# Kernel tuning notes

Measured on AMD Instinct MI355X. Metric: run time of the kernel, lower is better.

## Reference

```python
import jax, jax.numpy as jnp
import numpy as np

N_EV, N_CS, N_TR, N_ENV = 40000, 30000, 20000, 10000
N = N_EV + N_CS + N_TR + N_ENV  # 100000 nodes
E = 3_200_000                   # edges (avg degree 32)
FEAT, HID = 32, 64
N_GRAPHS, NPG = 100, 1000       # 100 graphs of 1000 nodes


def _p(k, shape, scale=0.1):
    return (jax.random.normal(k, shape, jnp.float32) * scale)


def setup_inputs() -> dict:
    key = jax.random.key(0)
    ks = jax.random.split(key, 24)
    inp = {
        'ev_features': jax.random.normal(ks[0], (N_EV, 6), jnp.float32),
        'cs_features': jax.random.normal(ks[1], (N_CS, 4), jnp.float32),
        'tr_features': jax.random.normal(ks[2], (N_TR, 2), jnp.float32),
        'env_features': jax.random.normal(ks[3], (N_ENV, 5), jnp.float32),
        'edge_index': jax.random.randint(ks[4], (2, E), 0, N, jnp.int32),
        'ev_indexes': jnp.arange(0, N_EV, dtype=jnp.int32),
        'cs_indexes': jnp.arange(N_EV, N_EV + N_CS, dtype=jnp.int32),
        'tr_indexes': jnp.arange(N_EV + N_CS, N_EV + N_CS + N_TR, dtype=jnp.int32),
        'env_indexes': jnp.arange(N - N_ENV, N, dtype=jnp.int32),
        'batch': (jnp.arange(N, dtype=jnp.int32) // NPG),
        'W_ev': _p(ks[5], (6, FEAT)),  'b_ev': _p(ks[6], (FEAT,)),
        'W_cs': _p(ks[7], (4, FEAT)),  'b_cs': _p(ks[8], (FEAT,)),
        'W_tr': _p(ks[9], (2, FEAT)),  'b_tr': _p(ks[10], (FEAT,)),
        'W_env': _p(ks[11], (5, FEAT)), 'b_env': _p(ks[12], (FEAT,)),
        'W1': _p(ks[13], (FEAT, HID)),      'b1': _p(ks[14], (HID,)),
        'W2': _p(ks[15], (HID, 2 * HID)),   'b2': _p(ks[16], (2 * HID,)),
        'W3': _p(ks[17], (2 * HID, HID)),   'b3': _p(ks[18], (HID,)),
    }
    return inp


def gcn_conv(x, src, dst, W, b):
    # PyG GCNConv: h = x W; add self-loops; symmetric norm D^-1/2 (A+I) D^-1/2; + bias
    h = x @ W
    ones_e = jnp.ones((src.shape[0],), h.dtype)
    deg = jnp.ones((N,), h.dtype).at[dst].add(ones_e)  # includes self-loop weight 1
    dinv = jax.lax.rsqrt(deg)
    norm = dinv[src] * dinv[dst]                       # [E]
    out = (h * (dinv * dinv)[:, None]).at[dst].add(h[src] * norm[:, None])
    return out + b


def reference(ev_features, cs_features, tr_features, env_features,
              edge_index, ev_indexes, cs_indexes, tr_indexes, env_indexes, batch,
              W_ev, b_ev, W_cs, b_cs, W_tr, b_tr, W_env, b_env,
              W1, b1, W2, b2, W3, b3):
    src, dst = edge_index[0], edge_index[1]
    x = jnp.zeros((N, FEAT), jnp.float32)
    x = x.at[ev_indexes].set(ev_features @ W_ev + b_ev)
    x = x.at[cs_indexes].set(cs_features @ W_cs + b_cs)
    x = x.at[tr_indexes].set(tr_features @ W_tr + b_tr)
    x = x.at[env_indexes].set(env_features @ W_env + b_env)

    x1 = gcn_conv(x, src, dst, W1, b1)                 # [N, HID]
    h = jax.nn.relu(x1)
    h = jax.nn.relu(gcn_conv(h, src, dst, W2, b2))     # [N, 2*HID]
    h = jax.nn.relu(gcn_conv(h, src, dst, W3, b3))     # [N, HID]
    h = h + x1                                          # residual

    # global_mean_pool over graph segments
    sums = jax.ops.segment_sum(h, batch, num_segments=N_GRAPHS)
    cnts = jax.ops.segment_sum(jnp.ones((N,), h.dtype), batch, num_segments=N_GRAPHS)
    return sums / cnts[:, None]
```

## Files before the change

### kernel.cpp

```cpp
#include <hip/hip_runtime.h>
#include <hip/hip_bf16.h>


#define THREADS 256
#define BINSHIFT 8
#define EPBA 4096
#define SCANCH 8

typedef __attribute__((ext_vector_type(8))) short short8;
typedef __attribute__((ext_vector_type(4))) float f32x4;

__device__ __forceinline__ unsigned bfpack2(float lo, float hi) {
    unsigned ul = __float_as_uint(lo);
    unsigned uh = __float_as_uint(hi);
    ul = (ul + 0x7fffu + ((ul >> 16) & 1u)) >> 16;
    uh = (uh + 0x7fffu + ((uh >> 16) & 1u)) & 0xffff0000u;
    return ul | uh;
}

__device__ __forceinline__ void bfacc(uint2 v, float& a0, float& a1,
                                      float& a2, float& a3) {
    a0 += __uint_as_float(v.x << 16);
    a1 += __uint_as_float(v.x & 0xffff0000u);
    a2 += __uint_as_float(v.y << 16);
    a3 += __uint_as_float(v.y & 0xffff0000u);
}

__device__ __forceinline__ short8 as_short8(uint4 u) {
    union { uint4 u; short8 s; } c; c.u = u; return c.s;
}

__global__ __launch_bounds__(THREADS)
void k_partcnt(const int* __restrict__ dst, int* __restrict__ counts,
               int nblk_part, int nb, int e) {
    extern __shared__ int h[];
    int t = threadIdx.x;
    for (int i = t; i < nb; i += THREADS) h[i] = 0;
    __syncthreads();
    int lo = blockIdx.x * EPBA;
    int hi = min(lo + EPBA, e);
    for (int i = lo + t; i < hi; i += THREADS)
        atomicAdd(&h[dst[i] >> BINSHIFT], 1);
    __syncthreads();
    for (int i = t; i < nb; i += THREADS)
        counts[(size_t)i * nblk_part + blockIdx.x] = h[i];
}

__global__ __launch_bounds__(THREADS)
void k_scanrows(int* __restrict__ counts, int* __restrict__ bintot, int nblk_part) {
    __shared__ int wsum[THREADS];
    int* row = counts + (size_t)blockIdx.x * nblk_part;
    int t = threadIdx.x;
    int base = t * SCANCH;
    int v[SCANCH];
    int s = 0;
#pragma unroll
    for (int k = 0; k < SCANCH; ++k) {
        v[k] = (base + k < nblk_part) ? row[base + k] : 0;
        s += v[k];
    }
    wsum[t] = s;
    __syncthreads();
    for (int off = 1; off < THREADS; off <<= 1) {
        int a = (t >= off) ? wsum[t - off] : 0;
        __syncthreads();
        wsum[t] += a;
        __syncthreads();
    }
    int run = wsum[t] - s;
#pragma unroll
    for (int k = 0; k < SCANCH; ++k) {
        int c = v[k];
        if (base + k < nblk_part) row[base + k] = run;
        run += c;
    }
    if (t == THREADS - 1) bintot[blockIdx.x] = run;
}

__global__ __launch_bounds__(512)
void k_binscan(const int* __restrict__ bintot, int* __restrict__ binptr,
               int nb, int e) {
    __shared__ int lds[512];
    int t = threadIdx.x;
    int v = (t < nb) ? bintot[t] : 0;
    lds[t] = v;
    __syncthreads();
    for (int off = 1; off < 512; off <<= 1) {
        int a = (t >= off) ? lds[t - off] : 0;
        __syncthreads();
        lds[t] += a;
        __syncthreads();
    }
    if (t < nb) binptr[t] = lds[t] - v;
    if (t == 0) binptr[nb] = e;
}

__global__ __launch_bounds__(THREADS)
void k_partwrite(const int* __restrict__ src, const int* __restrict__ dst,
                 const int* __restrict__ binptr, const int* __restrict__ counts,
                 int nblk_part, unsigned* __restrict__ pairs, int nb, int e) {
    extern __shared__ int smem[];
    int* base = smem;
    int* cnt  = smem + nb;
    int t = threadIdx.x;
    for (int i = t; i < nb; i += THREADS) {
        base[i] = binptr[i] + counts[(size_t)i * nblk_part + blockIdx.x];
        cnt[i] = 0;
    }
    __syncthreads();
    int lo = blockIdx.x * EPBA;
    int hi = min(lo + EPBA, e);
    for (int i = lo + t; i < hi; i += THREADS) {
        int s = src[i], d = dst[i];
        int b = d >> BINSHIFT;
        int pos = atomicAdd(&cnt[b], 1);
        pairs[base[b] + pos] = ((unsigned)s << BINSHIFT) | (unsigned)(d & ((1 << BINSHIFT) - 1));
    }
}

__global__ __launch_bounds__(THREADS)
void k_bincsr(const unsigned* __restrict__ pairs, const int* __restrict__ binptr,
              int* __restrict__ rowptr, float* __restrict__ dinv,
              int* __restrict__ srcs, int n, int nb, int e) {
    __shared__ int lcnt[256];
    __shared__ int lofs[256];
    int b = blockIdx.x, t = threadIdx.x;
    int e0 = binptr[b], e1 = binptr[b + 1];
    int n0 = b << BINSHIFT;
    constexpr unsigned NMASK = (1u << BINSHIFT) - 1u;
    lcnt[t] = 0;
    __syncthreads();
    for (int j = e0 + t; j < e1; j += THREADS)
        atomicAdd(&lcnt[pairs[j] & NMASK], 1);
    __syncthreads();
    int c = lcnt[t];
    lofs[t] = c;
    __syncthreads();
    for (int off = 1; off < THREADS; off <<= 1) {
        int a = (t >= off) ? lofs[t - off] : 0;
        __syncthreads();
        lofs[t] += a;
        __syncthreads();
    }
    int excl = lofs[t] - c;
    __syncthreads();
    lofs[t] = excl;
    int node = n0 + t;
    if (node < n) {
        rowptr[node] = e0 + excl;
        dinv[node] = rsqrtf((float)c + 1.0f);
    }
    if (b == nb - 1 && t == 0) rowptr[n] = e;
    __syncthreads();
    for (int j = e0 + t; j < e1; j += THREADS) {
        unsigned pp = pairs[j];
        int pos = e0 + atomicAdd(&lofs[pp & NMASK], 1);
        srcs[pos] = (int)(pp >> BINSHIFT);
    }
}

struct EmbedArgs {
    const float* f[4];
    const float* W[4];
    const float* b[4];
    const int*   idx[4];
    int cum[5];
    int Kv[4];
};

__global__ __launch_bounds__(THREADS)
void k_embed_all(EmbedArgs ea, const float* __restrict__ dinv,
                 unsigned* __restrict__ xb) {
    int g = blockIdx.x * THREADS + threadIdx.x;
    int row = g >> 4, cp = g & 15;
    if (row >= ea.cum[4]) return;
    int t = (row >= ea.cum[1]) + (row >= ea.cum[2]) + (row >= ea.cum[3]);
    int r = row - ea.cum[t];
    int K = ea.Kv[t];
    const float* f  = ea.f[t];
    const float* W  = ea.W[t];
    const float* bb = ea.b[t];
    int node = ea.idx[t][r];
    float dv = dinv[node];
    float a0 = bb[2 * cp], a1 = bb[2 * cp + 1];
    for (int k = 0; k < K; ++k) {
        float fv = f[r * K + k];
        a0 += fv * W[k * 32 + 2 * cp];
        a1 += fv * W[k * 32 + 2 * cp + 1];
    }
    xb[(size_t)node * 16 + cp] = bfpack2(dv * a0, dv * a1);
}

template <bool HASBIAS, bool OUTRELU, bool HASRES, bool OUTBF>
__global__ __launch_bounds__(THREADS)
void k_gather64(const unsigned* __restrict__ tblb, const int* __restrict__ rowptr,
                const int* __restrict__ srcs, const float* __restrict__ dinv,
                const float* __restrict__ bias, const unsigned* __restrict__ resid,
                void* __restrict__ outp, int n) {
    int gt = blockIdx.x * THREADS + threadIdx.x;
    int node = gt >> 6;
    int lane = threadIdx.x & 63;
    if (node >= n) return;
    int qw = lane >> 4, li = lane & 15;
    const uint2* t2 = reinterpret_cast<const uint2*>(tblb);
    float a0 = 0.f, a1 = 0.f, a2 = 0.f, a3 = 0.f;
    int beg = rowptr[node], end = rowptr[node + 1];
    int j = beg;
    for (; j + 32 <= end; j += 32) {
        int s[8];
#pragma unroll
        for (int u = 0; u < 8; ++u) s[u] = srcs[j + 4 * u + qw];
        uint2 v[8];
#pragma unroll
        for (int u = 0; u < 8; ++u) v[u] = t2[(size_t)s[u] * 16 + li];
#pragma unroll
        for (int u = 0; u < 8; ++u) bfacc(v[u], a0, a1, a2, a3);
    }
    for (; j + 8 <= end; j += 8) {
        int s0 = srcs[j + qw];
        int s1 = srcs[j + 4 + qw];
        uint2 v0 = t2[(size_t)s0 * 16 + li];
        uint2 v1 = t2[(size_t)s1 * 16 + li];
        bfacc(v0, a0, a1, a2, a3);
        bfacc(v1, a0, a1, a2, a3);
    }
    int rem = end - j;
    if (qw < rem) {
        uint2 v = t2[(size_t)srcs[j + qw] * 16 + li];
        bfacc(v, a0, a1, a2, a3);
    }
    if (qw + 4 < rem) {
        uint2 v = t2[(size_t)srcs[j + 4 + qw] * 16 + li];
        bfacc(v, a0, a1, a2, a3);
    }
    a0 += __shfl_down(a0, 32, 64); a1 += __shfl_down(a1, 32, 64);
    a2 += __shfl_down(a2, 32, 64); a3 += __shfl_down(a3, 32, 64);
    a0 += __shfl_down(a0, 16, 64); a1 += __shfl_down(a1, 16, 64);
    a2 += __shfl_down(a2, 16, 64); a3 += __shfl_down(a3, 16, 64);
    if (lane < 16) {
        uint2 sv = t2[(size_t)node * 16 + li];
        bfacc(sv, a0, a1, a2, a3);
        float dv = dinv[node];
        float r0 = dv * a0, r1 = dv * a1, r2 = dv * a2, r3 = dv * a3;
        if (HASBIAS) {
            float4 bv = *reinterpret_cast<const float4*>(bias + 4 * li);
            r0 += bv.x; r1 += bv.y; r2 += bv.z; r3 += bv.w;
        }
        if (OUTRELU) {
            r0 = fmaxf(r0, 0.f); r1 = fmaxf(r1, 0.f);
            r2 = fmaxf(r2, 0.f); r3 = fmaxf(r3, 0.f);
        }
        if (HASRES) {
            uint2 rv = reinterpret_cast<const uint2*>(resid)[(size_t)node * 16 + li];
            bfacc(rv, r0, r1, r2, r3);
        }
        if (OUTBF) {
            uint2 o = {bfpack2(r0, r1), bfpack2(r2, r3)};
            reinterpret_cast<uint2*>(outp)[(size_t)node * 16 + li] = o;
        } else {
            float4 o = {r0, r1, r2, r3};
            reinterpret_cast<float4*>(outp)[(size_t)node * 16 + li] = o;
        }
    }
}

__global__ __launch_bounds__(THREADS)
void k_gather32(const unsigned* __restrict__ tblb, const int* __restrict__ rowptr,
                const int* __restrict__ srcs, const float* __restrict__ dinv,
                unsigned* __restrict__ outb, int n) {
    int gt = blockIdx.x * THREADS + threadIdx.x;
    int node = gt >> 6;
    int lane = threadIdx.x & 63;
    if (node >= n) return;
    int og = lane >> 3, li = lane & 7;
    const uint2* t2 = reinterpret_cast<const uint2*>(tblb);
    float a0 = 0.f, a1 = 0.f, a2 = 0.f, a3 = 0.f;
    int beg = rowptr[node], end = rowptr[node + 1];
    int j = beg;
    for (; j + 32 <= end; j += 32) {
        int s[4];
#pragma unroll
        for (int u = 0; u < 4; ++u) s[u] = srcs[j + 8 * u + og];
        uint2 v[4];
#pragma unroll
        for (int u = 0; u < 4; ++u) v[u] = t2[(size_t)s[u] * 8 + li];
#pragma unroll
        for (int u = 0; u < 4; ++u) bfacc(v[u], a0, a1, a2, a3);
    }
    for (; j + 8 <= end; j += 8) {
        int s0 = srcs[j + og];
        uint2 v0 = t2[(size_t)s0 * 8 + li];
        bfacc(v0, a0, a1, a2, a3);
    }
    int rem = end - j;
    if (og < rem) {
        uint2 v = t2[(size_t)srcs[j + og] * 8 + li];
        bfacc(v, a0, a1, a2, a3);
    }
    a0 += __shfl_down(a0, 32, 64); a1 += __shfl_down(a1, 32, 64);
    a2 += __shfl_down(a2, 32, 64); a3 += __shfl_down(a3, 32, 64);
    a0 += __shfl_down(a0, 16, 64); a1 += __shfl_down(a1, 16, 64);
    a2 += __shfl_down(a2, 16, 64); a3 += __shfl_down(a3, 16, 64);
    a0 += __shfl_down(a0, 8, 64);  a1 += __shfl_down(a1, 8, 64);
    a2 += __shfl_down(a2, 8, 64);  a3 += __shfl_down(a3, 8, 64);
    if (lane < 8) {
        uint2 sv = t2[(size_t)node * 8 + li];
        bfacc(sv, a0, a1, a2, a3);
        float dv = dinv[node];
        uint2 o = {bfpack2(dv * a0, dv * a1), bfpack2(dv * a2, dv * a3)};
        reinterpret_cast<uint2*>(outb)[(size_t)node * 8 + li] = o;
    }
}

__global__ __launch_bounds__(THREADS)
void k_wprep_all(const float* __restrict__ W1, const float* __restrict__ W2,
                 const float* __restrict__ W3, unsigned* __restrict__ wt) {
    int g = blockIdx.x * THREADS + threadIdx.x;
    if (g < 1024) {
        int nn = g >> 4, kq = g & 15;
        wt[g] = bfpack2(W1[(size_t)(2 * kq) * 64 + nn], W1[(size_t)(2 * kq + 1) * 64 + nn]);
    } else if (g < 5120) {
        int gg = g - 1024;
        int nn = gg >> 5, kq = gg & 31;
        wt[g] = bfpack2(W2[(size_t)(2 * kq) * 128 + nn], W2[(size_t)(2 * kq + 1) * 128 + nn]);
    } else if (g < 9216) {
        int gg = g - 5120;
        int nn = gg >> 6, kq = gg & 63;
        wt[g] = bfpack2(W3[(size_t)(2 * kq) * 64 + nn], W3[(size_t)(2 * kq + 1) * 64 + nn]);
    }
}

template <int FIN, int FOUT, int EXTRA>
__global__ __launch_bounds__(THREADS)
void k_mmfa(const unsigned* __restrict__ xinb, const unsigned* __restrict__ wtb,
            const float* __restrict__ bias, const float* __restrict__ dinv,
            unsigned* __restrict__ outb, unsigned* __restrict__ outb2, int nrows) {
    constexpr int FH = FIN / 2;
    constexpr int KS = FIN / 32;
    constexpr int MT = FOUT / 16;
    int tid = threadIdx.x;
    int lane = tid & 63;
    int lg = lane >> 4, li = lane & 15;
    int node = blockIdx.x * 64 + (tid >> 6) * 16 + li;
    int nc = min(node, nrows - 1);

    const uint4* xr = reinterpret_cast<const uint4*>(xinb + (size_t)nc * FH);
    short8 bf[KS];
#pragma unroll
    for (int ks = 0; ks < KS; ++ks) bf[ks] = as_short8(xr[ks * 4 + lg]);

    f32x4 acc[MT];
#pragma unroll
    for (int mt = 0; mt < MT; ++mt) acc[mt] = (f32x4){0.f, 0.f, 0.f, 0.f};

#pragma unroll
    for (int ks = 0; ks < KS; ++ks) {
#pragma unroll
        for (int mt = 0; mt < MT; ++mt) {
            uint4 wu = *reinterpret_cast<const uint4*>(
                wtb + (size_t)(mt * 16 + li) * FH + ks * 16 + lg * 4);
            acc[mt] = __builtin_amdgcn_mfma_f32_16x16x32_bf16(
                as_short8(wu), bf[ks], acc[mt], 0, 0, 0);
        }
    }

    if (node >= nrows) return;
    float dv = (EXTRA != 3) ? dinv[node] : 0.f;
#pragma unroll
    for (int mt = 0; mt < MT; ++mt) {
        float v0 = acc[mt][0], v1 = acc[mt][1], v2 = acc[mt][2], v3 = acc[mt][3];
        int m0 = mt * 16 + lg * 4;
        if (EXTRA == 1 || EXTRA == 3) {
            float4 bv = *reinterpret_cast<const float4*>(bias + m0);
            v0 += bv.x; v1 += bv.y; v2 += bv.z; v3 += bv.w;
        }
        size_t ob = (size_t)node * (FOUT / 2) + mt * 8 + lg * 2;
        if (EXTRA == 1) {
            uint2 o = {bfpack2(v0, v1), bfpack2(v2, v3)};
            *reinterpret_cast<uint2*>(outb + ob) = o;
            uint2 s = {bfpack2(dv * fmaxf(v0, 0.f), dv * fmaxf(v1, 0.f)),
                       bfpack2(dv * fmaxf(v2, 0.f), dv * fmaxf(v3, 0.f))};
            *reinterpret_cast<uint2*>(outb2 + ob) = s;
        }
        if (EXTRA == 3) {
            uint2 o = {bfpack2(fmaxf(v0, 0.f), fmaxf(v1, 0.f)),
                       bfpack2(fmaxf(v2, 0.f), fmaxf(v3, 0.f))};
            *reinterpret_cast<uint2*>(outb + ob) = o;
        }
        if (EXTRA == 2) {
            uint2 o = {bfpack2(dv * v0, dv * v1), bfpack2(dv * v2, dv * v3)};
            *reinterpret_cast<uint2*>(outb + ob) = o;
        }
    }
}

__global__ __launch_bounds__(THREADS)
void k_pool(const unsigned* __restrict__ hb, const int* __restrict__ batch,
            float* __restrict__ sums, float* __restrict__ cnts, int n) {
    int c = threadIdx.x & 31;
    int rq = threadIdx.x >> 5;
    int r0 = blockIdx.x * THREADS;
    int rend = min(r0 + THREADS, n);
    int curg = -1;
    float a0 = 0.f, a1 = 0.f, cacc = 0.f;
    for (int r = r0 + rq; r < rend; r += 8) {
        int g = batch[r];
        if (g != curg) {
            if (curg >= 0) {
                atomicAdd(&sums[(size_t)curg * 64 + 2 * c], a0);
                atomicAdd(&sums[(size_t)curg * 64 + 2 * c + 1], a1);
                if (c == 0) atomicAdd(&cnts[curg], cacc);
            }
            curg = g; a0 = 0.f; a1 = 0.f; cacc = 0.f;
        }
        unsigned u = hb[(size_t)r * 32 + c];
        a0 += __uint_as_float(u << 16);
        a1 += __uint_as_float(u & 0xffff0000u);
        cacc += 1.f;
    }
    if (curg >= 0) {
        atomicAdd(&sums[(size_t)curg * 64 + 2 * c], a0);
        atomicAdd(&sums[(size_t)curg * 64 + 2 * c + 1], a1);
        if (c == 0) atomicAdd(&cnts[curg], cacc);
    }
}

__global__ __launch_bounds__(THREADS)
void k_div(const float* __restrict__ sums, const float* __restrict__ cnts,
           float* __restrict__ out, int total) {
    int i = blockIdx.x * THREADS + threadIdx.x;
    if (i < total) out[i] = sums[i] / cnts[i >> 6];
}

static inline size_t alignup(size_t v) { return (v + 255) & ~(size_t)255; }

extern "C" void kernel_launch(void* const* d_in, const int* in_sizes, int n_in,
                              void* d_out, int out_size, void* d_ws, size_t ws_size,
                              hipStream_t stream) {
    const float* ev_f  = (const float*)d_in[0];
    const float* cs_f  = (const float*)d_in[1];
    const float* tr_f  = (const float*)d_in[2];
    const float* env_f = (const float*)d_in[3];
    const int*   ei    = (const int*)d_in[4];
    const int*   ev_i  = (const int*)d_in[5];
    const int*   cs_i  = (const int*)d_in[6];
    const int*   tr_i  = (const int*)d_in[7];
    const int*   env_i = (const int*)d_in[8];
    const int*   batch = (const int*)d_in[9];
    const float* W_ev = (const float*)d_in[10]; const float* b_ev = (const float*)d_in[11];
    const float* W_cs = (const float*)d_in[12]; const float* b_cs = (const float*)d_in[13];
    const float* W_tr = (const float*)d_in[14]; const float* b_tr = (const float*)d_in[15];
    const float* W_env= (const float*)d_in[16]; const float* b_env= (const float*)d_in[17];
    const float* W1 = (const float*)d_in[18]; const float* b1 = (const float*)d_in[19];
    const float* W2 = (const float*)d_in[20]; const float* b2 = (const float*)d_in[21];
    const float* W3 = (const float*)d_in[22]; const float* b3 = (const float*)d_in[23];

    const int E_ = in_sizes[4] / 2;
    const int N_ = in_sizes[9];
    const int n_ev  = in_sizes[5];
    const int n_cs  = in_sizes[6];
    const int n_tr  = in_sizes[7];
    const int n_env = in_sizes[8];
    const int ngr   = out_size / 64;

    const int* e_src = ei;
    const int* e_dst = ei + E_;

    const int NB   = (N_ + (1 << BINSHIFT) - 1) >> BINSHIFT;
    const int ablk = (E_ + EPBA - 1) / EPBA;

    char* p = (char*)d_ws;
    int*      counts = (int*)p;      p += alignup((size_t)NB * ablk * 4);
    int*      bintot = (int*)p;      p += alignup((size_t)NB * 4);
    int*      binptr = (int*)p;      p += alignup(((size_t)NB + 1) * 4);
    int*      rowptr = (int*)p;      p += alignup(((size_t)N_ + 1) * 4);
    float*    dinv   = (float*)p;    p += alignup((size_t)N_ * 4);
    int*      srcs   = (int*)p;      p += alignup((size_t)E_ * 4);
    unsigned* xb     = (unsigned*)p; p += alignup((size_t)N_ * 16 * 4);
    unsigned* x1b    = (unsigned*)p; p += alignup((size_t)N_ * 32 * 4);
    unsigned* x1s_bf = (unsigned*)p; p += alignup((size_t)N_ * 32 * 4);
    unsigned* aggb   = (unsigned*)p; p += alignup((size_t)N_ * 32 * 4);
    unsigned* hA     = (unsigned*)p; p += alignup((size_t)N_ * 64 * 4);
    unsigned* t3s_bf = (unsigned*)p; p += alignup((size_t)N_ * 32 * 4);
    unsigned* hfb    = (unsigned*)p; p += alignup((size_t)N_ * 32 * 4);
    unsigned* wt     = (unsigned*)p; p += alignup((size_t)9216 * 4);
    float*    sums   = (float*)p;    p += alignup((size_t)ngr * 64 * 4);
    float*    cnts   = (float*)p;    p += alignup((size_t)ngr * 4);

    unsigned* w1t = wt;
    unsigned* w2t = wt + 1024;
    unsigned* w3t = wt + 5120;

    unsigned* pairs = hA;

    const int nblk  = (N_ + THREADS - 1) / THREADS;
    const int mfblk = (N_ + 63) / 64;
    const int gblk  = ((size_t)N_ * 64 + THREADS - 1) / THREADS;

    hipMemsetAsync(sums, 0, (size_t)ngr * 64 * 4, stream);
    hipMemsetAsync(cnts, 0, (size_t)ngr * 4, stream);

    k_partcnt<<<ablk, THREADS, (size_t)NB * 4, stream>>>(e_dst, counts, ablk, NB, E_);
    k_scanrows<<<NB, THREADS, 0, stream>>>(counts, bintot, ablk);
    k_binscan<<<1, 512, 0, stream>>>(bintot, binptr, NB, E_);
    k_partwrite<<<ablk, THREADS, (size_t)NB * 8, stream>>>(e_src, e_dst, binptr, counts, ablk, pairs, NB, E_);
    k_bincsr<<<NB, THREADS, 0, stream>>>(pairs, binptr, rowptr, dinv, srcs, N_, NB, E_);

    k_wprep_all<<<(9216 + THREADS - 1) / THREADS, THREADS, 0, stream>>>(W1, W2, W3, wt);

    EmbedArgs ea;
    ea.f[0] = ev_f;  ea.f[1] = cs_f;  ea.f[2] = tr_f;  ea.f[3] = env_f;
    ea.W[0] = W_ev;  ea.W[1] = W_cs;  ea.W[2] = W_tr;  ea.W[3] = W_env;
    ea.b[0] = b_ev;  ea.b[1] = b_cs;  ea.b[2] = b_tr;  ea.b[3] = b_env;
    ea.idx[0] = ev_i; ea.idx[1] = cs_i; ea.idx[2] = tr_i; ea.idx[3] = env_i;
    ea.cum[0] = 0;
    ea.cum[1] = n_ev;
    ea.cum[2] = n_ev + n_cs;
    ea.cum[3] = n_ev + n_cs + n_tr;
    ea.cum[4] = n_ev + n_cs + n_tr + n_env;
    ea.Kv[0] = in_sizes[0] / n_ev;
    ea.Kv[1] = in_sizes[1] / n_cs;
    ea.Kv[2] = in_sizes[2] / n_tr;
    ea.Kv[3] = in_sizes[3] / n_env;
    k_embed_all<<<((size_t)ea.cum[4] * 16 + THREADS - 1) / THREADS, THREADS, 0, stream>>>(ea, dinv, xb);

    k_gather32<<<gblk, THREADS, 0, stream>>>(xb, rowptr, srcs, dinv, aggb, N_);
    k_mmfa<32, 64, 1><<<mfblk, THREADS, 0, stream>>>(aggb, w1t, b1, dinv, x1b, x1s_bf, N_);

    k_gather64<false, false, false, true><<<gblk, THREADS, 0, stream>>>(
        x1s_bf, rowptr, srcs, dinv, nullptr, nullptr, aggb, N_);
    k_mmfa<64, 128, 3><<<mfblk, THREADS, 0, stream>>>(aggb, w2t, b2, nullptr, hA, nullptr, N_);

    k_mmfa<128, 64, 2><<<mfblk, THREADS, 0, stream>>>(hA, w3t, nullptr, dinv, t3s_bf, nullptr, N_);
    k_gather64<true, true, true, true><<<gblk, THREADS, 0, stream>>>(
        t3s_bf, rowptr, srcs, dinv, b3, x1b, hfb, N_);

    k_pool<<<nblk, THREADS, 0, stream>>>(hfb, batch, sums, cnts, N_);
    k_div<<<(out_size + THREADS - 1) / THREADS, THREADS, 0, stream>>>(sums, cnts, (float*)d_out, out_size);
}
```

Baseline: 359.4 us.

## Stage partition writes in LDS for coalesced bin output; shrink gather unroll

The partition-write kernel now builds a local histogram and scan per block, stages the packed (src,dst) pairs in shared memory grouped by bin, and then writes each bin's run to global memory contiguously with one wave per bin. This replaces scattered per-edge global writes with coalesced runs. The edges-per-block count doubles to 8192, which needs 32KB of LDS plus extra syncs and may lower occupancy. The gather kernels also cut their inner unroll from 32 to 16 edges per iteration, which reduces register pressure but leaves fewer loads in flight.

```diff
diff --git a/kernel.cpp b/kernel.cpp
--- a/kernel.cpp
+++ b/kernel.cpp
@@ -4,8 +4,9 @@
 
 #define THREADS 256
 #define BINSHIFT 8
-#define EPBA 4096
+#define EPBA 8192
 #define SCANCH 8
+#define NBMAX 416
 
 typedef __attribute__((ext_vector_type(8))) short short8;
 typedef __attribute__((ext_vector_type(4))) float f32x4;
@@ -99,22 +100,51 @@
 void k_partwrite(const int* __restrict__ src, const int* __restrict__ dst,
                  const int* __restrict__ binptr, const int* __restrict__ counts,
                  int nblk_part, unsigned* __restrict__ pairs, int nb, int e) {
-    extern __shared__ int smem[];
-    int* base = smem;
-    int* cnt  = smem + nb;
+    __shared__ int hist[NBMAX];
+    __shared__ int lbase[NBMAX];
+    __shared__ int gbase[NBMAX];
+    __shared__ int cur[NBMAX];
+    __shared__ int wsum[THREADS];
+    __shared__ unsigned stage[EPBA];
     int t = threadIdx.x;
-    for (int i = t; i < nb; i += THREADS) {
-        base[i] = binptr[i] + counts[(size_t)i * nblk_part + blockIdx.x];
-        cnt[i] = 0;
-    }
+    for (int i = t; i < nb; i += THREADS) hist[i] = 0;
     __syncthreads();
     int lo = blockIdx.x * EPBA;
     int hi = min(lo + EPBA, e);
+    for (int i = lo + t; i < hi; i += THREADS)
+        atomicAdd(&hist[dst[i] >> BINSHIFT], 1);
+    __syncthreads();
+    int v0 = (2 * t < nb) ? hist[2 * t] : 0;
+    int v1 = (2 * t + 1 < nb) ? hist[2 * t + 1] : 0;
+    int s = v0 + v1;
+    wsum[t] = s;
+    __syncthreads();
+    for (int off = 1; off < THREADS; off <<= 1) {
+        int a = (t >= off) ? wsum[t - off] : 0;
+        __syncthreads();
+        wsum[t] += a;
+        __syncthreads();
+    }
+    int excl = wsum[t] - s;
+    if (2 * t < nb) { lbase[2 * t] = excl; cur[2 * t] = excl; }
+    if (2 * t + 1 < nb) { lbase[2 * t + 1] = excl + v0; cur[2 * t + 1] = excl + v0; }
+    for (int i = t; i < nb; i += THREADS)
+        gbase[i] = binptr[i] + counts[(size_t)i * nblk_part + blockIdx.x];
+    __syncthreads();
     for (int i = lo + t; i < hi; i += THREADS) {
-        int s = src[i], d = dst[i];
+        int s2 = src[i], d = dst[i];
         int b = d >> BINSHIFT;
-        int pos = atomicAdd(&cnt[b], 1);
-        pairs[base[b] + pos] = ((unsigned)s << BINSHIFT) | (unsigned)(d & ((1 << BINSHIFT) - 1));
+        int pos = atomicAdd(&cur[b], 1);
+        stage[pos] = ((unsigned)s2 << BINSHIFT) | (unsigned)(d & ((1 << BINSHIFT) - 1));
+    }
+    __syncthreads();
+    int wid = t >> 6, lane = t & 63;
+    for (int b = wid; b < nb; b += (THREADS / 64)) {
+        int n = hist[b];
+        int lb = lbase[b];
+        int gb = gbase[b];
+        for (int k = lane; k < n; k += 64)
+            pairs[gb + k] = stage[lb + k];
     }
 }
 
@@ -206,21 +236,25 @@
     float a0 = 0.f, a1 = 0.f, a2 = 0.f, a3 = 0.f;
     int beg = rowptr[node], end = rowptr[node + 1];
     int j = beg;
-    for (; j + 32 <= end; j += 32) {
-        int s[8];
-#pragma unroll
-        for (int u = 0; u < 8; ++u) s[u] = srcs[j + 4 * u + qw];
-        uint2 v[8];
-#pragma unroll
-        for (int u = 0; u < 8; ++u) v[u] = t2[(size_t)s[u] * 16 + li];
-#pragma unroll
-        for (int u = 0; u < 8; ++u) bfacc(v[u], a0, a1, a2, a3);
+    for (; j + 16 <= end; j += 16) {
+        int i0 = srcs[j + qw];
+        int i1 = srcs[j + 4 + qw];
+        int i2 = srcs[j + 8 + qw];
+        int i3 = srcs[j + 12 + qw];
+        uint2 v0 = t2[(size_t)i0 * 16 + li];
+        uint2 v1 = t2[(size_t)i1 * 16 + li];
+        uint2 v2 = t2[(size_t)i2 * 16 + li];
+        uint2 v3 = t2[(size_t)i3 * 16 + li];
+        bfacc(v0, a0, a1, a2, a3);
+        bfacc(v1, a0, a1, a2, a3);
+        bfacc(v2, a0, a1, a2, a3);
+        bfacc(v3, a0, a1, a2, a3);
     }
     for (; j + 8 <= end; j += 8) {
-        int s0 = srcs[j + qw];
-        int s1 = srcs[j + 4 + qw];
-        uint2 v0 = t2[(size_t)s0 * 16 + li];
-        uint2 v1 = t2[(size_t)s1 * 16 + li];
+        int i0 = srcs[j + qw];
+        int i1 = srcs[j + 4 + qw];
+        uint2 v0 = t2[(size_t)i0 * 16 + li];
+        uint2 v1 = t2[(size_t)i1 * 16 + li];
         bfacc(v0, a0, a1, a2, a3);
         bfacc(v1, a0, a1, a2, a3);
     }
@@ -277,19 +311,17 @@
     float a0 = 0.f, a1 = 0.f, a2 = 0.f, a3 = 0.f;
     int beg = rowptr[node], end = rowptr[node + 1];
     int j = beg;
-    for (; j + 32 <= end; j += 32) {
-        int s[4];
-#pragma unroll
-        for (int u = 0; u < 4; ++u) s[u] = srcs[j + 8 * u + og];
-        uint2 v[4];
-#pragma unroll
-        for (int u = 0; u < 4; ++u) v[u] = t2[(size_t)s[u] * 8 + li];
-#pragma unroll
-        for (int u = 0; u < 4; ++u) bfacc(v[u], a0, a1, a2, a3);
+    for (; j + 16 <= end; j += 16) {
+        int i0 = srcs[j + og];
+        int i1 = srcs[j + 8 + og];
+        uint2 v0 = t2[(size_t)i0 * 8 + li];
+        uint2 v1 = t2[(size_t)i1 * 8 + li];
+        bfacc(v0, a0, a1, a2, a3);
+        bfacc(v1, a0, a1, a2, a3);
     }
     for (; j + 8 <= end; j += 8) {
-        int s0 = srcs[j + og];
-        uint2 v0 = t2[(size_t)s0 * 8 + li];
+        int i0 = srcs[j + og];
+        uint2 v0 = t2[(size_t)i0 * 8 + li];
         bfacc(v0, a0, a1, a2, a3);
     }
     int rem = end - j;
@@ -503,7 +535,7 @@
     k_partcnt<<<ablk, THREADS, (size_t)NB * 4, stream>>>(e_dst, counts, ablk, NB, E_);
     k_scanrows<<<NB, THREADS, 0, stream>>>(counts, bintot, ablk);
     k_binscan<<<1, 512, 0, stream>>>(bintot, binptr, NB, E_);
-    k_partwrite<<<ablk, THREADS, (size_t)NB * 8, stream>>>(e_src, e_dst, binptr, counts, ablk, pairs, NB, E_);
+    k_partwrite<<<ablk, THREADS, 0, stream>>>(e_src, e_dst, binptr, counts, ablk, pairs, NB, E_);
     k_bincsr<<<NB, THREADS, 0, stream>>>(pairs, binptr, rowptr, dinv, srcs, N_, NB, E_);
 
     k_wprep_all<<<(9216 + THREADS - 1) / THREADS, THREADS, 0, stream>>>(W1, W2, W3, wt);
```

Measured after the change: 353.3 us. No clear change (-1.7%).
